# Kernel tuning notes

Measured on AMD Instinct MI355X. Metric: run time of the kernel, lower is better.

Reference implementation:

```python
import jax, jax.numpy as jnp
import numpy as np

# kernel / loss hyperparameters (from base_params)
FIT_SIGMA = 1.0
FIT_L = 1.0
MMD_SIGMA = 1.0
MMD_L = 2.0
REG_LAMBDA = 0.01

N, D = 8192, 16


def setup_inputs() -> dict:
    key = jax.random.key(0)
    k1, k2, k3 = jax.random.split(key, 3)
    X = jax.random.normal(k1, (N, D), dtype=jnp.float32)
    Y = jax.random.normal(k2, (N, D), dtype=jnp.float32)
    Lam = jax.random.normal(k3, (N, D), dtype=jnp.float32)  # nn.init.normal_ on zeros(N,d)
    return {"X": X, "Y": Y, "Lam": Lam}


def _rbf_gram(X, sigma, l):
    # k(xi, xj) = sigma^2 * exp(-||xi - xj||^2 / (2 l^2)), vectorized over all pairs
    sq = jnp.sum(X * X, axis=1)                      # [N]
    d2 = sq[:, None] + sq[None, :] - 2.0 * (X @ X.T)  # [N, N] squared distances
    d2 = jnp.maximum(d2, 0.0)
    return (sigma ** 2) * jnp.exp(-d2 / (2.0 * l ** 2))


def reference(X, Y, Lam):
    fit_kXX = _rbf_gram(X, FIT_SIGMA, FIT_L)   # [N, N]
    mmd_kXX = _rbf_gram(X, MMD_SIGMA, MMD_L)   # [N, N]
    diff = fit_kXX @ Lam - Y                   # [N, d]
    # trace(diff^T K diff) = sum(diff * (K @ diff))
    loss_fit = jnp.sum(diff * (mmd_kXX @ diff))
    loss_reg = REG_LAMBDA * jnp.sum(Lam * (fit_kXX @ Lam))
    return loss_fit + loss_reg
```

## Files before the change

### kernel.cpp

```cpp
#include <hip/hip_runtime.h>

#define NPTS 8192
#define DIM  16

constexpr int BLK = 256;
constexpr int NIB = NPTS / BLK;

#define REG_LAMBDA 0.01f
#define C1 1.2011224087864498f
#define C2 0.6005612043932249f

typedef _Float16 h4 __attribute__((ext_vector_type(4)));
typedef float    f4 __attribute__((ext_vector_type(4)));

#define MFMA16(a, b, c) __builtin_amdgcn_mfma_f32_16x16x16f16((a), (b), (c), 0, 0, 0)

#if __has_builtin(__builtin_amdgcn_exp2f)
#define EXP2(x) __builtin_amdgcn_exp2f(x)
#else
#define EXP2(x) exp2f(x)
#endif

__device__ __forceinline__ float dot4(float4 a, float4 b) {
  return fmaf(a.x, b.x, fmaf(a.y, b.y, fmaf(a.z, b.z, a.w * b.w)));
}

__device__ __forceinline__ float block_sum(float v, float* wbuf) {
#pragma unroll
  for (int o = 32; o > 0; o >>= 1) v += __shfl_down(v, o, 64);
  const int lane = threadIdx.x & 63;
  const int wid  = threadIdx.x >> 6;
  __syncthreads();
  if (lane == 0) wbuf[wid] = v;
  __syncthreads();
  float s = 0.f;
  if (threadIdx.x == 0) {
#pragma unroll
    for (int w = 0; w < BLK / 64; ++w) s += wbuf[w];
  }
  return s;
}

__global__ __launch_bounds__(BLK) void k_prep(
    const float4* __restrict__ Xv, const float4* __restrict__ Lv,
    _Float16* __restrict__ Xh1, _Float16* __restrict__ Xh2,
    _Float16* __restrict__ LamT,
    float* __restrict__ csq1, float* __restrict__ csq2,
    float* __restrict__ accums) {
  if (blockIdx.x == 0 && threadIdx.x < 4) accums[threadIdx.x] = 0.f;
  const int i = blockIdx.x * BLK + threadIdx.x;
  float sq1 = 0.f, sq2 = 0.f;
  h4* x1 = (h4*)(Xh1 + (size_t)i * DIM);
  h4* x2 = (h4*)(Xh2 + (size_t)i * DIM);
#pragma unroll
  for (int q = 0; q < 4; ++q) {
    const float4 v = Xv[(size_t)i * 4 + q];
    h4 a = {(_Float16)(C1 * v.x), (_Float16)(C1 * v.y),
            (_Float16)(C1 * v.z), (_Float16)(C1 * v.w)};
    h4 b = {(_Float16)(C2 * v.x), (_Float16)(C2 * v.y),
            (_Float16)(C2 * v.z), (_Float16)(C2 * v.w)};
    x1[q] = a; x2[q] = b;
#pragma unroll
    for (int t = 0; t < 4; ++t) {
      const float fa = (float)a[t], fb = (float)b[t];
      sq1 = fmaf(fa, fa, sq1);
      sq2 = fmaf(fb, fb, sq2);
    }
    const float4 l = Lv[(size_t)i * 4 + q];
    LamT[(size_t)(4 * q + 0) * NPTS + i] = (_Float16)l.x;
    LamT[(size_t)(4 * q + 1) * NPTS + i] = (_Float16)l.y;
    LamT[(size_t)(4 * q + 2) * NPTS + i] = (_Float16)l.z;
    LamT[(size_t)(4 * q + 3) * NPTS + i] = (_Float16)l.w;
  }
  csq1[i] = -0.5f * sq1;
  csq2[i] = -0.5f * sq2;
}

__global__ __launch_bounds__(BLK) void k_pass1(
    const _Float16* __restrict__ Xh1, const _Float16* __restrict__ LamT,
    const float* __restrict__ csq1, _Float16* __restrict__ Upart, int span) {
  const int lane = threadIdx.x & 63;
  const int w    = threadIdx.x >> 6;
  const int l16  = lane & 15;
  const int quad = lane >> 4;

  const int i0 = blockIdx.x * 256 + w * 64;
  h4 bxi[4];
  float ci[4];
#pragma unroll
  for (int t = 0; t < 4; ++t) {
    bxi[t] = *(const h4*)(Xh1 + (size_t)(i0 + 16 * t + l16) * DIM + quad * 4);
    ci[t]  = csq1[i0 + 16 * t + l16];
  }
  const _Float16* blrow = LamT + (size_t)l16 * NPTS;

  f4 U[4] = {{0.f, 0.f, 0.f, 0.f}, {0.f, 0.f, 0.f, 0.f},
             {0.f, 0.f, 0.f, 0.f}, {0.f, 0.f, 0.f, 0.f}};
  const int jbeg = blockIdx.y * span;
  const int jend = jbeg + span;
#pragma unroll 4
  for (int j0 = jbeg; j0 < jend; j0 += 16) {
    const h4 axj = *(const h4*)(Xh1 + (size_t)(j0 + l16) * DIM + quad * 4);
    const float4 cjf = *(const float4*)(csq1 + j0 + quad * 4);
    const h4 bl = *(const h4*)(blrow + j0 + quad * 4);
#pragma unroll
    for (int t = 0; t < 4; ++t) {
      const f4 cc = {cjf.x + ci[t], cjf.y + ci[t], cjf.z + ci[t], cjf.w + ci[t]};
      const f4 p = MFMA16(axj, bxi[t], cc);
      h4 ap;
#pragma unroll
      for (int r = 0; r < 4; ++r) ap[r] = (_Float16)EXP2(p[r]);
      U[t] = MFMA16(ap, bl, U[t]);
    }
  }

  _Float16* dst = Upart + ((size_t)blockIdx.y * NPTS + i0) * DIM;
#pragma unroll
  for (int t = 0; t < 4; ++t)
#pragma unroll
    for (int r = 0; r < 4; ++r)
      dst[(16 * t + quad * 4 + r) * DIM + l16] = (_Float16)U[t][r];
}

__global__ __launch_bounds__(BLK) void k_reduce(
    const _Float16* __restrict__ Upart, const float4* __restrict__ Yv,
    const float4* __restrict__ Lv, _Float16* __restrict__ Dh,
    float* __restrict__ accums, int jc) {
  __shared__ float wred[BLK / 64];
  const int t = blockIdx.x * BLK + threadIdx.x;
  const int i = t >> 2, q = t & 3;
  float4 u = {0.f, 0.f, 0.f, 0.f};
  for (int c = 0; c < jc; ++c) {
    const h4 p = *(const h4*)(Upart + ((size_t)c * NPTS + i) * DIM + q * 4);
    u.x += (float)p[0]; u.y += (float)p[1];
    u.z += (float)p[2]; u.w += (float)p[3];
  }
  const float4 y = Yv[(size_t)i * 4 + q];
  h4 d = {(_Float16)(u.x - y.x), (_Float16)(u.y - y.y),
          (_Float16)(u.z - y.z), (_Float16)(u.w - y.w)};
  *(h4*)(Dh + (size_t)i * DIM + q * 4) = d;
  const float regp = dot4(Lv[(size_t)i * 4 + q], u);
  const float rtot = block_sum(regp, wred);
  if (threadIdx.x == 0) unsafeAtomicAdd(&accums[1], rtot);
}

__global__ __launch_bounds__(BLK) void k_pass2(
    const _Float16* __restrict__ Xh2, const _Float16* __restrict__ Dh,
    const float* __restrict__ csq2, float* __restrict__ accums) {
  __shared__ float wred[BLK / 64];
  const int bi   = blockIdx.x;
  const int k    = blockIdx.y >> 1;
  const int half = blockIdx.y & 1;
  if (k == 16 && bi >= 16) return;
  const int bj = (bi + k) & 31;
  const float weight = (k == 0) ? 1.f : 2.f;

  const int lane = threadIdx.x & 63;
  const int w    = threadIdx.x >> 6;
  const int l16  = lane & 15;
  const int quad = lane >> 4;
  const f4 fz = {0.f, 0.f, 0.f, 0.f};

  const int i0 = bi * 256 + w * 64;
  h4 ax[4], ad[4];
  float4 cif[4];
#pragma unroll
  for (int t = 0; t < 4; ++t) {
    ax[t] = *(const h4*)(Xh2 + (size_t)(i0 + 16 * t + l16) * DIM + quad * 4);
    ad[t] = *(const h4*)(Dh  + (size_t)(i0 + 16 * t + l16) * DIM + quad * 4);
    cif[t] = *(const float4*)(csq2 + i0 + 16 * t + quad * 4);
  }

  float s = 0.f;
  const int jbeg = bj * 256 + half * 128;
  const int jend = jbeg + 128;
#pragma unroll 4
  for (int j0 = jbeg; j0 < jend; j0 += 16) {
    const h4 bx = *(const h4*)(Xh2 + (size_t)(j0 + l16) * DIM + quad * 4);
    const h4 bd = *(const h4*)(Dh  + (size_t)(j0 + l16) * DIM + quad * 4);
    const float cj = csq2[j0 + l16];
#pragma unroll
    for (int t = 0; t < 4; ++t) {
      const f4 cc = {cif[t].x + cj, cif[t].y + cj, cif[t].z + cj, cif[t].w + cj};
      const f4 dx = MFMA16(ax[t], bx, cc);
      const f4 dd = MFMA16(ad[t], bd, fz);
#pragma unroll
      for (int r = 0; r < 4; ++r) s = fmaf(EXP2(dx[r]), dd[r], s);
    }
  }

  const float stot = block_sum(s * weight, wred);
  if (threadIdx.x == 0) unsafeAtomicAdd(&accums[0], stot);
}

__global__ void k_final(const float* __restrict__ accums, float* __restrict__ out) {
  out[0] = accums[0] + REG_LAMBDA * accums[1];
}

extern "C" void kernel_launch(void* const* d_in, const int* in_sizes, int n_in,
                              void* d_out, int out_size, void* d_ws, size_t ws_size,
                              hipStream_t stream) {
  const float4* Xv = (const float4*)d_in[0];
  const float4* Yv = (const float4*)d_in[1];
  const float4* Lv = (const float4*)d_in[2];
  float* out = (float*)d_out;

  char* base = (char*)d_ws;
  _Float16* Xh1  = (_Float16*)(base);
  _Float16* Xh2  = (_Float16*)(base + 256 * 1024);
  _Float16* LamT = (_Float16*)(base + 512 * 1024);
  _Float16* Dh   = (_Float16*)(base + 768 * 1024);
  float*    csq1 = (float*)(base + 1024 * 1024);
  float*    csq2 = (float*)(base + 1056 * 1024);
  float*    accums = (float*)(base + 1088 * 1024);
  _Float16* Upart  = (_Float16*)(base + 1088 * 1024 + 256);
  const size_t fixed = 1088 * 1024 + 256;

  int jc = 32;
  while (jc > 1 && fixed + (size_t)jc * NPTS * DIM * 2 > ws_size) jc >>= 1;
  const int span1 = NPTS / jc;

  k_prep<<<NIB, BLK, 0, stream>>>(Xv, Lv, Xh1, Xh2, LamT, csq1, csq2, accums);
  k_pass1<<<dim3(NPTS / 256, jc), BLK, 0, stream>>>(Xh1, LamT, csq1, Upart, span1);
  k_reduce<<<NPTS * 4 / BLK, BLK, 0, stream>>>(Upart, Yv, Lv, Dh, accums, jc);
  k_pass2<<<dim3(32, 34), BLK, 0, stream>>>(Xh2, Dh, csq2, accums);
  k_final<<<1, 1, 0, stream>>>(accums, out);
}
```

Baseline: 111.1 us.

## Fold squared-norm bias into padded K=32 MFMA and pre-block Lambda fragments

The -0.5*||x||^2 terms now live in extra padded feature columns (as hi/lo fp16 pairs times ones), so a single 16x16x32 MFMA yields the full exponent. This removes the per-tile bias loads and vector adds that fed the accumulator in both passes. Lambda is stored in a fragment-blocked layout so each lane does one contiguous load, exp results are packed with cvt_pkrtz, and the reduce kernel handles 8 values per thread. The cost is doubled X storage and bandwidth, since rows are padded to 32 halfs, and some bias precision risk from the fp16 hi/lo split.

```diff
diff --git a/kernel.cpp b/kernel.cpp
--- a/kernel.cpp
+++ b/kernel.cpp
@@ -2,6 +2,7 @@
 
 #define NPTS 8192
 #define DIM  16
+#define DPAD 32
 
 constexpr int BLK = 256;
 constexpr int NIB = NPTS / BLK;
@@ -11,19 +12,17 @@
 #define C2 0.6005612043932249f
 
 typedef _Float16 h4 __attribute__((ext_vector_type(4)));
+typedef _Float16 h8 __attribute__((ext_vector_type(8)));
 typedef float    f4 __attribute__((ext_vector_type(4)));
 
 #define MFMA16(a, b, c) __builtin_amdgcn_mfma_f32_16x16x16f16((a), (b), (c), 0, 0, 0)
+#define MFMA32(a, b, c) __builtin_amdgcn_mfma_f32_16x16x32_f16((a), (b), (c), 0, 0, 0)
 
 #if __has_builtin(__builtin_amdgcn_exp2f)
 #define EXP2(x) __builtin_amdgcn_exp2f(x)
 #else
 #define EXP2(x) exp2f(x)
 #endif
-
-__device__ __forceinline__ float dot4(float4 a, float4 b) {
-  return fmaf(a.x, b.x, fmaf(a.y, b.y, fmaf(a.z, b.z, a.w * b.w)));
-}
 
 __device__ __forceinline__ float block_sum(float v, float* wbuf) {
 #pragma unroll
@@ -43,15 +42,13 @@
 
 __global__ __launch_bounds__(BLK) void k_prep(
     const float4* __restrict__ Xv, const float4* __restrict__ Lv,
-    _Float16* __restrict__ Xh1, _Float16* __restrict__ Xh2,
-    _Float16* __restrict__ LamT,
-    float* __restrict__ csq1, float* __restrict__ csq2,
-    float* __restrict__ accums) {
+    _Float16* __restrict__ XA1, _Float16* __restrict__ XB1,
+    _Float16* __restrict__ XA2, _Float16* __restrict__ XB2,
+    _Float16* __restrict__ LamB, float* __restrict__ accums) {
   if (blockIdx.x == 0 && threadIdx.x < 4) accums[threadIdx.x] = 0.f;
   const int i = blockIdx.x * BLK + threadIdx.x;
   float sq1 = 0.f, sq2 = 0.f;
-  h4* x1 = (h4*)(Xh1 + (size_t)i * DIM);
-  h4* x2 = (h4*)(Xh2 + (size_t)i * DIM);
+  h4 a1[4], a2[4];
 #pragma unroll
   for (int q = 0; q < 4; ++q) {
     const float4 v = Xv[(size_t)i * 4 + q];
@@ -59,57 +56,83 @@
             (_Float16)(C1 * v.z), (_Float16)(C1 * v.w)};
     h4 b = {(_Float16)(C2 * v.x), (_Float16)(C2 * v.y),
             (_Float16)(C2 * v.z), (_Float16)(C2 * v.w)};
-    x1[q] = a; x2[q] = b;
+    a1[q] = a; a2[q] = b;
 #pragma unroll
     for (int t = 0; t < 4; ++t) {
       const float fa = (float)a[t], fb = (float)b[t];
       sq1 = fmaf(fa, fa, sq1);
       sq2 = fmaf(fb, fb, sq2);
     }
+  }
+  const float c1 = -0.5f * sq1, c2 = -0.5f * sq2;
+  const _Float16 c1h = (_Float16)c1;
+  const _Float16 c1l = (_Float16)(c1 - (float)c1h);
+  const _Float16 c2h = (_Float16)c2;
+  const _Float16 c2l = (_Float16)(c2 - (float)c2h);
+  const _Float16 one = (_Float16)1.f;
+  const _Float16 zer = (_Float16)0.f;
+  const h4 z4 = {zer, zer, zer, zer};
+
+  h4* rA1 = (h4*)(XA1 + (size_t)i * DPAD);
+  h4* rB1 = (h4*)(XB1 + (size_t)i * DPAD);
+  h4* rA2 = (h4*)(XA2 + (size_t)i * DPAD);
+  h4* rB2 = (h4*)(XB2 + (size_t)i * DPAD);
+#pragma unroll
+  for (int q = 0; q < 4; ++q) {
+    rA1[q] = a1[q]; rB1[q] = a1[q];
+    rA2[q] = a2[q]; rB2[q] = a2[q];
+  }
+  const h4 padA1 = {one, one, c1h, c1l};
+  const h4 padB1 = {c1h, c1l, one, one};
+  const h4 padA2 = {one, one, c2h, c2l};
+  const h4 padB2 = {c2h, c2l, one, one};
+  rA1[4] = padA1; rB1[4] = padB1;
+  rA2[4] = padA2; rB2[4] = padB2;
+#pragma unroll
+  for (int q = 5; q < 8; ++q) {
+    rA1[q] = z4; rB1[q] = z4; rA2[q] = z4; rB2[q] = z4;
+  }
+
+  _Float16* lb = LamB + (size_t)(i >> 4) * 256 + ((i >> 2) & 3) * 64 + (i & 3);
+#pragma unroll
+  for (int q = 0; q < 4; ++q) {
     const float4 l = Lv[(size_t)i * 4 + q];
-    LamT[(size_t)(4 * q + 0) * NPTS + i] = (_Float16)l.x;
-    LamT[(size_t)(4 * q + 1) * NPTS + i] = (_Float16)l.y;
-    LamT[(size_t)(4 * q + 2) * NPTS + i] = (_Float16)l.z;
-    LamT[(size_t)(4 * q + 3) * NPTS + i] = (_Float16)l.w;
-  }
-  csq1[i] = -0.5f * sq1;
-  csq2[i] = -0.5f * sq2;
+    lb[(4 * q + 0) * 4] = (_Float16)l.x;
+    lb[(4 * q + 1) * 4] = (_Float16)l.y;
+    lb[(4 * q + 2) * 4] = (_Float16)l.z;
+    lb[(4 * q + 3) * 4] = (_Float16)l.w;
+  }
 }
 
 __global__ __launch_bounds__(BLK) void k_pass1(
-    const _Float16* __restrict__ Xh1, const _Float16* __restrict__ LamT,
-    const float* __restrict__ csq1, _Float16* __restrict__ Upart, int span) {
+    const _Float16* __restrict__ XA1, const _Float16* __restrict__ XB1,
+    const _Float16* __restrict__ LamB, _Float16* __restrict__ Upart, int span) {
   const int lane = threadIdx.x & 63;
   const int w    = threadIdx.x >> 6;
   const int l16  = lane & 15;
   const int quad = lane >> 4;
 
   const int i0 = blockIdx.x * 256 + w * 64;
-  h4 bxi[4];
-  float ci[4];
-#pragma unroll
-  for (int t = 0; t < 4; ++t) {
-    bxi[t] = *(const h4*)(Xh1 + (size_t)(i0 + 16 * t + l16) * DIM + quad * 4);
-    ci[t]  = csq1[i0 + 16 * t + l16];
-  }
-  const _Float16* blrow = LamT + (size_t)l16 * NPTS;
-
-  f4 U[4] = {{0.f, 0.f, 0.f, 0.f}, {0.f, 0.f, 0.f, 0.f},
-             {0.f, 0.f, 0.f, 0.f}, {0.f, 0.f, 0.f, 0.f}};
+  h8 bxi[4];
+#pragma unroll
+  for (int t = 0; t < 4; ++t)
+    bxi[t] = *(const h8*)(XB1 + (size_t)(i0 + 16 * t + l16) * DPAD + quad * 8);
+
+  const f4 fz = {0.f, 0.f, 0.f, 0.f};
+  f4 U[4] = {fz, fz, fz, fz};
   const int jbeg = blockIdx.y * span;
   const int jend = jbeg + span;
 #pragma unroll 4
   for (int j0 = jbeg; j0 < jend; j0 += 16) {
-    const h4 axj = *(const h4*)(Xh1 + (size_t)(j0 + l16) * DIM + quad * 4);
-    const float4 cjf = *(const float4*)(csq1 + j0 + quad * 4);
-    const h4 bl = *(const h4*)(blrow + j0 + quad * 4);
+    const h8 axj = *(const h8*)(XA1 + (size_t)(j0 + l16) * DPAD + quad * 8);
+    const h4 bl  = *(const h4*)(LamB + (size_t)(j0 >> 4) * 256 + lane * 4);
 #pragma unroll
     for (int t = 0; t < 4; ++t) {
-      const f4 cc = {cjf.x + ci[t], cjf.y + ci[t], cjf.z + ci[t], cjf.w + ci[t]};
-      const f4 p = MFMA16(axj, bxi[t], cc);
+      const f4 p = MFMA32(axj, bxi[t], fz);
+      const auto lo = __builtin_amdgcn_cvt_pkrtz(EXP2(p[0]), EXP2(p[1]));
+      const auto hi = __builtin_amdgcn_cvt_pkrtz(EXP2(p[2]), EXP2(p[3]));
       h4 ap;
-#pragma unroll
-      for (int r = 0; r < 4; ++r) ap[r] = (_Float16)EXP2(p[r]);
+      ap[0] = lo[0]; ap[1] = lo[1]; ap[2] = hi[0]; ap[3] = hi[1];
       U[t] = MFMA16(ap, bl, U[t]);
     }
   }
@@ -128,25 +151,35 @@
     float* __restrict__ accums, int jc) {
   __shared__ float wred[BLK / 64];
   const int t = blockIdx.x * BLK + threadIdx.x;
-  const int i = t >> 2, q = t & 3;
-  float4 u = {0.f, 0.f, 0.f, 0.f};
+  const int i = t >> 1, hf = t & 1;
+  float u[8] = {0.f, 0.f, 0.f, 0.f, 0.f, 0.f, 0.f, 0.f};
   for (int c = 0; c < jc; ++c) {
-    const h4 p = *(const h4*)(Upart + ((size_t)c * NPTS + i) * DIM + q * 4);
-    u.x += (float)p[0]; u.y += (float)p[1];
-    u.z += (float)p[2]; u.w += (float)p[3];
-  }
-  const float4 y = Yv[(size_t)i * 4 + q];
-  h4 d = {(_Float16)(u.x - y.x), (_Float16)(u.y - y.y),
-          (_Float16)(u.z - y.z), (_Float16)(u.w - y.w)};
-  *(h4*)(Dh + (size_t)i * DIM + q * 4) = d;
-  const float regp = dot4(Lv[(size_t)i * 4 + q], u);
+    const h8 p = *(const h8*)(Upart + ((size_t)c * NPTS + i) * DIM + hf * 8);
+#pragma unroll
+    for (int r = 0; r < 8; ++r) u[r] += (float)p[r];
+  }
+  const float4 y0 = Yv[(size_t)i * 4 + 2 * hf];
+  const float4 y1 = Yv[(size_t)i * 4 + 2 * hf + 1];
+  h8 d;
+  d[0] = (_Float16)(u[0] - y0.x); d[1] = (_Float16)(u[1] - y0.y);
+  d[2] = (_Float16)(u[2] - y0.z); d[3] = (_Float16)(u[3] - y0.w);
+  d[4] = (_Float16)(u[4] - y1.x); d[5] = (_Float16)(u[5] - y1.y);
+  d[6] = (_Float16)(u[6] - y1.z); d[7] = (_Float16)(u[7] - y1.w);
+  *(h8*)(Dh + (size_t)i * DIM + hf * 8) = d;
+  const float4 l0 = Lv[(size_t)i * 4 + 2 * hf];
+  const float4 l1 = Lv[(size_t)i * 4 + 2 * hf + 1];
+  float regp = 0.f;
+  regp = fmaf(l0.x, u[0], regp); regp = fmaf(l0.y, u[1], regp);
+  regp = fmaf(l0.z, u[2], regp); regp = fmaf(l0.w, u[3], regp);
+  regp = fmaf(l1.x, u[4], regp); regp = fmaf(l1.y, u[5], regp);
+  regp = fmaf(l1.z, u[6], regp); regp = fmaf(l1.w, u[7], regp);
   const float rtot = block_sum(regp, wred);
   if (threadIdx.x == 0) unsafeAtomicAdd(&accums[1], rtot);
 }
 
 __global__ __launch_bounds__(BLK) void k_pass2(
-    const _Float16* __restrict__ Xh2, const _Float16* __restrict__ Dh,
-    const float* __restrict__ csq2, float* __restrict__ accums) {
+    const _Float16* __restrict__ XA2, const _Float16* __restrict__ XB2,
+    const _Float16* __restrict__ Dh, float* __restrict__ accums) {
   __shared__ float wred[BLK / 64];
   const int bi   = blockIdx.x;
   const int k    = blockIdx.y >> 1;
@@ -162,13 +195,12 @@
   const f4 fz = {0.f, 0.f, 0.f, 0.f};
 
   const int i0 = bi * 256 + w * 64;
-  h4 ax[4], ad[4];
-  float4 cif[4];
+  h8 ax[4];
+  h4 ad[4];
 #pragma unroll
   for (int t = 0; t < 4; ++t) {
-    ax[t] = *(const h4*)(Xh2 + (size_t)(i0 + 16 * t + l16) * DIM + quad * 4);
+    ax[t] = *(const h8*)(XA2 + (size_t)(i0 + 16 * t + l16) * DPAD + quad * 8);
     ad[t] = *(const h4*)(Dh  + (size_t)(i0 + 16 * t + l16) * DIM + quad * 4);
-    cif[t] = *(const float4*)(csq2 + i0 + 16 * t + quad * 4);
   }
 
   float s = 0.f;
@@ -176,13 +208,11 @@
   const int jend = jbeg + 128;
 #pragma unroll 4
   for (int j0 = jbeg; j0 < jend; j0 += 16) {
-    const h4 bx = *(const h4*)(Xh2 + (size_t)(j0 + l16) * DIM + quad * 4);
+    const h8 bx = *(const h8*)(XB2 + (size_t)(j0 + l16) * DPAD + quad * 8);
     const h4 bd = *(const h4*)(Dh  + (size_t)(j0 + l16) * DIM + quad * 4);
-    const float cj = csq2[j0 + l16];
 #pragma unroll
     for (int t = 0; t < 4; ++t) {
-      const f4 cc = {cif[t].x + cj, cif[t].y + cj, cif[t].z + cj, cif[t].w + cj};
-      const f4 dx = MFMA16(ax[t], bx, cc);
+      const f4 dx = MFMA32(ax[t], bx, fz);
       const f4 dd = MFMA16(ad[t], bd, fz);
 #pragma unroll
       for (int r = 0; r < 4; ++r) s = fmaf(EXP2(dx[r]), dd[r], s);
@@ -206,23 +236,23 @@
   float* out = (float*)d_out;
 
   char* base = (char*)d_ws;
-  _Float16* Xh1  = (_Float16*)(base);
-  _Float16* Xh2  = (_Float16*)(base + 256 * 1024);
-  _Float16* LamT = (_Float16*)(base + 512 * 1024);
-  _Float16* Dh   = (_Float16*)(base + 768 * 1024);
-  float*    csq1 = (float*)(base + 1024 * 1024);
-  float*    csq2 = (float*)(base + 1056 * 1024);
-  float*    accums = (float*)(base + 1088 * 1024);
-  _Float16* Upart  = (_Float16*)(base + 1088 * 1024 + 256);
-  const size_t fixed = 1088 * 1024 + 256;
+  _Float16* XA1  = (_Float16*)(base);
+  _Float16* XB1  = (_Float16*)(base + 512 * 1024);
+  _Float16* XA2  = (_Float16*)(base + 1024 * 1024);
+  _Float16* XB2  = (_Float16*)(base + 1536 * 1024);
+  _Float16* LamB = (_Float16*)(base + 2048 * 1024);
+  _Float16* Dh   = (_Float16*)(base + 2304 * 1024);
+  float*    accums = (float*)(base + 2560 * 1024);
+  _Float16* Upart  = (_Float16*)(base + 2560 * 1024 + 256);
+  const size_t fixed = 2560 * 1024 + 256;
 
   int jc = 32;
   while (jc > 1 && fixed + (size_t)jc * NPTS * DIM * 2 > ws_size) jc >>= 1;
   const int span1 = NPTS / jc;
 
-  k_prep<<<NIB, BLK, 0, stream>>>(Xv, Lv, Xh1, Xh2, LamT, csq1, csq2, accums);
-  k_pass1<<<dim3(NPTS / 256, jc), BLK, 0, stream>>>(Xh1, LamT, csq1, Upart, span1);
-  k_reduce<<<NPTS * 4 / BLK, BLK, 0, stream>>>(Upart, Yv, Lv, Dh, accums, jc);
-  k_pass2<<<dim3(32, 34), BLK, 0, stream>>>(Xh2, Dh, csq2, accums);
+  k_prep<<<NIB, BLK, 0, stream>>>(Xv, Lv, XA1, XB1, XA2, XB2, LamB, accums);
+  k_pass1<<<dim3(NPTS / 256, jc), BLK, 0, stream>>>(XA1, XB1, LamB, Upart, span1);
+  k_reduce<<<NPTS * 2 / BLK, BLK, 0, stream>>>(Upart, Yv, Lv, Dh, accums, jc);
+  k_pass2<<<dim3(32, 34), BLK, 0, stream>>>(XA2, XB2, Dh, accums);
   k_final<<<1, 1, 0, stream>>>(accums, out);
 }
```

Result: no change. 111.6 us (+0.5%).
